# Performance work log

Measured on AMD Instinct MI355X. Metric: run time of the kernel, lower is better.

The kernel has to match this reference:

```python
import jax, jax.numpy as jnp
import numpy as np

B, N = 4, 2466  # batch, vertex count (Pixel2Mesh stage-3 mesh)
IMG = 224.0


def _vertex_align(feat_maps, pos):
    """Bilinear-style gather of image features at projected vertex locations.
    feat_maps: list of [B,C,S,S]; pos: [B,N,3]. Returns [B,N,sum(C)]."""
    z = pos[..., 2]
    h = jnp.clip(248.0 * (pos[..., 1] / z) + 111.5, 0.0, 223.0)
    w = jnp.clip(248.0 * (pos[..., 0] / (-z)) + 111.5, 0.0, 223.0)
    outs = []
    for f in feat_maps:
        S = f.shape[-1]
        x = h / (IMG / S)
        y = w / (IMG / S)
        x1 = jnp.floor(x).astype(jnp.int32)
        x2 = jnp.minimum(jnp.ceil(x).astype(jnp.int32), S - 1)
        y1 = jnp.floor(y).astype(jnp.int32)
        y2 = jnp.minimum(jnp.ceil(y).astype(jnp.int32), S - 1)
        xi = x.astype(jnp.int32)  # trunc == floor since x >= 0
        yi = y.astype(jnp.int32)

        def gat(fm, xs, ys):  # fm [C,S,S], xs/ys [N] -> [N,C]
            return fm[:, xs, ys].T

        g = jax.vmap(gat)
        w11 = ((x2 - xi) * (y2 - yi)).astype(f.dtype)[..., None]
        w12 = ((x2 - xi) * (yi - y1)).astype(f.dtype)[..., None]
        w21 = ((xi - x1) * (y2 - yi)).astype(f.dtype)[..., None]
        w22 = ((xi - x1) * (yi - y1)).astype(f.dtype)[..., None]
        outs.append(w11 * g(f, x1, y1) + w21 * g(f, x2, y1)
                    + w12 * g(f, x1, y2) + w22 * g(f, x2, y2))
    return jnp.concatenate(outs, axis=-1)


def _graph_conv(x, adj, w0, w1):
    # relu(X @ w0 + A @ (X @ w1))
    return jax.nn.relu(x @ w0 + jnp.einsum('bmn,bnc->bmc', adj, x @ w1))


def _res_graph_conv(x, adj, pw, pb, w00, w01, w10, w11):
    skip = x @ pw + pb
    out = _graph_conv(x, adj, w00, w01)
    out = _graph_conv(out, adj, w10, w11)
    return skip + out


def _forward(conv2_3, conv3_4, conv4_6, conv5_3, vertex_positions, vertex_features,
             vertex_adjacency, lin_w, lin_b,
             r0_pw, r0_pb, r0_w00, r0_w01, r0_w10, r0_w11,
             r1_pw, r1_pb, r1_w00, r1_w01, r1_w10, r1_w11,
             r2_pw, r2_pb, r2_w00, r2_w01, r2_w10, r2_w11,
             gf_w0, gf_w1):
    aligned = _vertex_align([conv2_3, conv3_4, conv4_6, conv5_3], vertex_positions)  # [B,N,3840]
    proj = aligned @ lin_w + lin_b  # [B,N,128]
    x = jnp.concatenate([proj, vertex_features, vertex_positions], axis=-1)  # [B,N,259]
    x = _res_graph_conv(x, vertex_adjacency, r0_pw, r0_pb, r0_w00, r0_w01, r0_w10, r0_w11)
    x = _res_graph_conv(x, vertex_adjacency, r1_pw, r1_pb, r1_w00, r1_w01, r1_w10, r1_w11)
    x = _res_graph_conv(x, vertex_adjacency, r2_pw, r2_pb, r2_w00, r2_w01, r2_w10, r2_w11)
    offset = jnp.tanh(_graph_conv(x, vertex_adjacency, gf_w0, gf_w1))  # [B,N,3]
    return vertex_positions + offset


def setup_inputs() -> dict:
    key = jax.random.key(0)
    ks = jax.random.split(key, 40)
    inp = {
        "conv2_3": jax.random.normal(ks[0], (B, 256, 56, 56), jnp.float32),
        "conv3_4": jax.random.normal(ks[1], (B, 512, 28, 28), jnp.float32),
        "conv4_6": jax.random.normal(ks[2], (B, 1024, 14, 14), jnp.float32),
        "conv5_3": jax.random.normal(ks[3], (B, 2048, 7, 7), jnp.float32),
        "vertex_positions": jax.random.normal(ks[4], (B, N, 3), jnp.float32),
        "vertex_features": jax.random.normal(ks[5], (B, N, 128), jnp.float32),
        # sparse 0/1 adjacency stored dense (the torch module uses dense bmm)
        "vertex_adjacency": (jax.random.uniform(ks[6], (B, N, N)) < 0.003).astype(jnp.float32),
    }

    def u(k, shape, fan):
        b = 1.0 / np.sqrt(fan)
        return jax.random.uniform(k, shape, jnp.float32, -b, b)

    specs = [("lin_w", (3840, 128), 3840), ("lin_b", (128,), 3840)]
    for j, ci in enumerate([259, 128, 128]):
        p = f"r{j}_"
        specs += [(p + "pw", (ci, 128), ci), (p + "pb", (128,), ci),
                  (p + "w00", (ci, 128), ci), (p + "w01", (ci, 128), ci),
                  (p + "w10", (128, 128), 128), (p + "w11", (128, 128), 128)]
    specs += [("gf_w0", (128, 3), 128), ("gf_w1", (128, 3), 128)]
    for i, (name, shape, fan) in enumerate(specs):
        inp[name] = u(ks[7 + i], shape, fan)
    return inp


def reference(conv2_3, conv3_4, conv4_6, conv5_3, vertex_positions, vertex_features,
              vertex_adjacency, lin_w, lin_b,
              r0_pw, r0_pb, r0_w00, r0_w01, r0_w10, r0_w11,
              r1_pw, r1_pb, r1_w00, r1_w01, r1_w10, r1_w11,
              r2_pw, r2_pb, r2_w00, r2_w01, r2_w10, r2_w11,
              gf_w0, gf_w1):
    return _forward(conv2_3, conv3_4, conv4_6, conv5_3, vertex_positions, vertex_features,
                    vertex_adjacency, lin_w, lin_b,
                    r0_pw, r0_pb, r0_w00, r0_w01, r0_w10, r0_w11,
                    r1_pw, r1_pb, r1_w00, r1_w01, r1_w10, r1_w11,
                    r2_pw, r2_pb, r2_w00, r2_w01, r2_w10, r2_w11,
                    gf_w0, gf_w1)
```

## Files before the change

### kernel.cpp

```cpp
#include <hip/hip_runtime.h>
#include <cmath>

#define B_   4
#define N_   2466
#define R_   (B_*N_)
#define ELLW 96

typedef _Float16 f16x8 __attribute__((ext_vector_type(8)));
typedef _Float16 f16x4 __attribute__((ext_vector_type(4)));
typedef __attribute__((ext_vector_type(4))) float f32x4;

__device__ __forceinline__ unsigned short f16_bits(float x) {
  union { _Float16 h; unsigned short u; } c;
  c.h = (_Float16)x;
  return c.u;
}

struct WMats { const float* p[15]; };


__global__ __launch_bounds__(256) void k_pre(
    const float* __restrict__ c2, const float* __restrict__ c3,
    const float* __restrict__ c4, const float* __restrict__ c5,
    unsigned short* __restrict__ t0, unsigned short* __restrict__ t1,
    unsigned short* __restrict__ t2, unsigned short* __restrict__ t3,
    const float* __restrict__ adj, int* __restrict__ cols, int* __restrict__ cnts,
    const float* __restrict__ lin_w,
    unsigned short* __restrict__ whf,
    WMats wm,
    unsigned short* __restrict__ wrf) {
  __shared__ float t[64][66];
  int bid = blockIdx.x;
  int tid = threadIdx.x;
  if (bid < 1584) {
    const float* in; unsigned short* out; int C, P, npb, ncb, rem;
    if (bid < 784)       { in = c2; out = t0; C = 256;  P = 3136; npb = 49; ncb = 4;  rem = bid; }
    else if (bid < 1200) { in = c3; out = t1; C = 512;  P = 784;  npb = 13; ncb = 8;  rem = bid - 784; }
    else if (bid < 1456) { in = c4; out = t2; C = 1024; P = 196;  npb = 4;  ncb = 16; rem = bid - 1200; }
    else                 { in = c5; out = t3; C = 2048; P = 49;   npb = 1;  ncb = 32; rem = bid - 1456; }
    int pb = rem % npb; int tq = rem / npb; int cb = tq % ncb; int b = tq / ncb;
    int c0 = cb * 64, p0 = pb * 64;
    #pragma unroll
    for (int i = 0; i < 8; i++) {
      int e = tid + i * 256;
      int c = e >> 5, f2 = e & 31;
      int p = p0 + f2 * 2;
      float2 v = make_float2(0.f, 0.f);
      const float* src = in + ((size_t)b * C + (c0 + c)) * P + p;
      if (p + 1 < P)      v = *(const float2*)src;
      else if (p < P)     v.x = *src;
      *(float2*)&t[c][f2 * 2] = v;
    }
    __syncthreads();
    int jj = tid & 15, c4i = jj * 4;
    #pragma unroll
    for (int pass = 0; pass < 4; pass++) {
      int pp = pass * 16 + (tid >> 4);
      int px = p0 + pp;
      if (px < P) {
        ushort4 o;
        o.x = f16_bits(t[c4i + 0][pp]);
        o.y = f16_bits(t[c4i + 1][pp]);
        o.z = f16_bits(t[c4i + 2][pp]);
        o.w = f16_bits(t[c4i + 3][pp]);
        *(ushort4*)&out[((size_t)b * P + px) * C + c0 + c4i] = o;
      }
    }
  } else if (bid < 4050) {
    int wave = tid >> 6, lane = tid & 63;
    int row = (bid - 1584) * 4 + wave;
    const float* Ar = adj + (size_t)row * N_;
    int* cp = cols + (size_t)row * ELLW;
    unsigned long long below = (lane == 63) ? 0xFFFFFFFFFFFFFFFFull >> 1
                                            : ((1ull << lane) - 1ull);
    float4 v[10];
    #pragma unroll
    for (int i0 = 0; i0 < 10; i0++) {
      int j0 = i0 * 256 + lane * 4;
      if (j0 + 3 < N_) {
        v[i0] = *(const float4*)&Ar[j0];
      } else {
        v[i0] = make_float4(0.f, 0.f, 0.f, 0.f);
        if (j0     < N_) v[i0].x = Ar[j0];
        if (j0 + 1 < N_) v[i0].y = Ar[j0+1];
        if (j0 + 2 < N_) v[i0].z = Ar[j0+2];
      }
    }
    int base = 0;
    #pragma unroll
    for (int i0 = 0; i0 < 10; i0++) {
      int j0 = i0 * 256 + lane * 4;
      bool nz0 = (j0     < N_) && (v[i0].x != 0.f);
      bool nz1 = (j0 + 1 < N_) && (v[i0].y != 0.f);
      bool nz2 = (j0 + 2 < N_) && (v[i0].z != 0.f);
      bool nz3 = (j0 + 3 < N_) && (v[i0].w != 0.f);
      unsigned long long m0 = __ballot(nz0);
      unsigned long long m1 = __ballot(nz1);
      unsigned long long m2 = __ballot(nz2);
      unsigned long long m3 = __ballot(nz3);
      int pre = __popcll(m0 & below) + __popcll(m1 & below)
              + __popcll(m2 & below) + __popcll(m3 & below);
      int p0 = base + pre;
      int p1 = p0 + (nz0 ? 1 : 0);
      int p2 = p1 + (nz1 ? 1 : 0);
      int p3 = p2 + (nz2 ? 1 : 0);
      if (nz0 && p0 < ELLW) cp[p0] = j0;
      if (nz1 && p1 < ELLW) cp[p1] = j0 + 1;
      if (nz2 && p2 < ELLW) cp[p2] = j0 + 2;
      if (nz3 && p3 < ELLW) cp[p3] = j0 + 3;
      base += __popcll(m0) + __popcll(m1) + __popcll(m2) + __popcll(m3);
    }
    if (lane == 0) cnts[row] = (base > ELLW) ? ELLW : base;
  } else if (bid < 4530) {
    int b = bid - 4050;
    int e0 = (b * 256 + tid) * 4;
    #pragma unroll
    for (int u = 0; u < 4; u++) {
      int e = e0 + u;
      int j = e & 7;
      int lane = (e >> 3) & 63;
      int nt = (e >> 9) & 7;
      int slab = e >> 12;
      int k = slab * 32 + ((lane >> 4) << 3) + j;
      int n = nt * 16 + (lane & 15);
      whf[e] = f16_bits(lin_w[(size_t)k * 128 + n]);
    }
  } else {
    int b = bid - 4530;
    int e0 = (b * 256 + tid) * 4;
    #pragma unroll
    for (int u = 0; u < 4; u++) {
      int e = e0 + u;
      int rb, mat, rem, K;
      if (e < 143360) {
        rb = 0;
        if (e < 110592) { mat = e / 36864; rem = e - mat * 36864; K = 259; }
        else { int tt = e - 110592; mat = 3 + tt / 16384; rem = tt & 16383; K = 128; }
      } else {
        int tt = e - 143360;
        rb = 1 + tt / 81920;
        int r2 = tt % 81920;
        mat = r2 / 16384; rem = r2 & 16383; K = 128;
      }
      int j = rem & 7, lane = (rem >> 3) & 63, nt = (rem >> 9) & 7, slab = rem >> 12;
      int k = slab * 32 + ((lane >> 4) << 3) + j;
      int n = nt * 16 + (lane & 15);
      float x = (k < K) ? wm.p[rb * 5 + mat][(size_t)k * 128 + n] : 0.f;
      wrf[e] = f16_bits(x);
    }
  }
}

__global__ __launch_bounds__(256) void k_align_mfma(
    const unsigned short* __restrict__ tr0, const unsigned short* __restrict__ tr1,
    const unsigned short* __restrict__ tr2, const unsigned short* __restrict__ tr3,
    const float* __restrict__ pos,
    const unsigned short* __restrict__ whf,
    unsigned short* __restrict__ part, int kchunk) {
  int tid  = threadIdx.x;
  int wave = tid >> 6, lane = tid & 63;
  int q    = lane >> 4, l15 = lane & 15;
  int m0   = blockIdx.x * 128;
  int s    = blockIdx.y;

  int zero[2][4]; int base[2][4];
  #pragma unroll
  for (int u = 0; u < 2; u++) {
    int mrow = m0 + (wave * 2 + u) * 16 + l15;
    int rowc = (mrow < R_) ? mrow : 0;
    int b = rowc / N_;
    float px = pos[rowc*3+0], py = pos[rowc*3+1], pz = pos[rowc*3+2];
    float hh = fminf(fmaxf(248.f*(py/pz)    + 111.5f, 0.f), 223.f);
    float wc = fminf(fmaxf(248.f*(px/(-pz)) + 111.5f, 0.f), 223.f);
    const int Sarr[4] = {56, 28, 14, 7};
    const int Carr[4] = {256, 512, 1024, 2048};
    #pragma unroll
    for (int sc = 0; sc < 4; sc++) {
      int S = Sarr[sc], C = Carr[sc];
      float dv = 224.f / (float)S;
      float x = hh / dv, y = wc / dv;
      int x1 = (int)floorf(x), y1 = (int)floorf(y);
      int x2 = min((int)ceilf(x), S - 1), y2 = min((int)ceilf(y), S - 1);
      int w = (x2 - x1) * (y2 - y1);
      zero[u][sc] = (mrow >= R_) || (w == 0);
      base[u][sc] = (b * S * S + x1 * S + y1) * C;
    }
  }

  f32x4 acc[2][8];
  #pragma unroll
  for (int u = 0; u < 2; u++)
    #pragma unroll
    for (int nt = 0; nt < 8; nt++) acc[u][nt] = (f32x4){0.f, 0.f, 0.f, 0.f};

  const f16x8* BH = (const f16x8*)whf;

  int kbeg = s * kchunk, kend = kbeg + kchunk;
  #pragma unroll 1
  for (int k0 = kbeg; k0 < kend; k0 += 32) {
    const unsigned short* tr; int off, sI;
    if (k0 < 256)       { tr = tr0; off = 0;    sI = 0; }
    else if (k0 < 768)  { tr = tr1; off = 256;  sI = 1; }
    else if (k0 < 1792) { tr = tr2; off = 768;  sI = 2; }
    else                { tr = tr3; off = 1792; sI = 3; }

    f16x8 af[2];
    #pragma unroll
    for (int u = 0; u < 2; u++) {
      af[u] = *(const f16x8*)(tr + base[u][sI] + (k0 - off) + q * 8);
      if (zero[u][sI]) af[u] = (f16x8)(_Float16)0;
    }

    int slab = k0 >> 5;
    f16x8 Bh[8];
    #pragma unroll
    for (int nt = 0; nt < 8; nt++)
      Bh[nt] = BH[(size_t)(slab * 8 + nt) * 64 + lane];
    #pragma unroll
    for (int nt = 0; nt < 8; nt++) {
      acc[0][nt] = __builtin_amdgcn_mfma_f32_16x16x32_f16(af[0], Bh[nt], acc[0][nt], 0, 0, 0);
      acc[1][nt] = __builtin_amdgcn_mfma_f32_16x16x32_f16(af[1], Bh[nt], acc[1][nt], 0, 0, 0);
    }
  }

  #pragma unroll
  for (int u = 0; u < 2; u++)
    #pragma unroll
    for (int nt = 0; nt < 8; nt++)
      #pragma unroll
      for (int r = 0; r < 4; r++) {
        int row = m0 + (wave * 2 + u) * 16 + q * 4 + r;
        if (row < R_)
          part[((size_t)s * R_ + row) * 128 + nt * 16 + l15] = f16_bits(acc[u][nt][r]);
      }
}

__global__ __launch_bounds__(256) void k_reduce(
    const unsigned short* __restrict__ part, const float* __restrict__ lin_b,
    const float* __restrict__ vf, const float* __restrict__ pos,
    unsigned short* __restrict__ xcat, int nsplit) {
  int grp = threadIdx.x >> 5, ln = threadIdx.x & 31;
  int row = blockIdx.x * 8 + grp;
  float4 acc = ((const float4*)lin_b)[ln];
  const f16x4* p4 = (const f16x4*)part;
  for (int s = 0; s < nsplit; s++) {
    f16x4 pv = p4[((size_t)s * R_ + row) * 32 + ln];
    acc.x += (float)pv[0]; acc.y += (float)pv[1];
    acc.z += (float)pv[2]; acc.w += (float)pv[3];
  }
  ushort4* xr = (ushort4*)(xcat + (size_t)row * 288);
  ushort4 o;
  o.x = f16_bits(acc.x); o.y = f16_bits(acc.y);
  o.z = f16_bits(acc.z); o.w = f16_bits(acc.w);
  xr[ln] = o;
  float4 vv = ((const float4*)vf)[(size_t)row * 32 + ln];
  o.x = f16_bits(vv.x); o.y = f16_bits(vv.y);
  o.z = f16_bits(vv.z); o.w = f16_bits(vv.w);
  xr[32 + ln] = o;
  if (ln < 8) {
    ushort4 z = make_ushort4(0, 0, 0, 0);
    if (ln == 0) {
      z.x = f16_bits(pos[(size_t)row * 3 + 0]);
      z.y = f16_bits(pos[(size_t)row * 3 + 1]);
      z.z = f16_bits(pos[(size_t)row * 3 + 2]);
    }
    xr[64 + ln] = z;
  }
}

template<int SLABS>
__global__ __launch_bounds__(256) void k_gemm_mfma(
    const unsigned short* __restrict__ X, int ldx,
    const unsigned short* __restrict__ wf,
    int matStride, const float* __restrict__ pb,
    unsigned short* __restrict__ o0, unsigned short* __restrict__ o1,
    unsigned short* __restrict__ o2) {
  int tid = threadIdx.x;
  int wave = tid >> 6, lane = tid & 63;
  int q = lane >> 4, l15 = lane & 15;
  int which = blockIdx.y;
  int m0 = blockIdx.x * 64;
  int mrow = m0 + wave * 16 + l15;
  int rowc = (mrow < R_) ? mrow : (R_ - 1);
  const unsigned short* xrow = X + (size_t)rowc * ldx + q * 8;

  const f16x8* BH = (const f16x8*)(wf + (size_t)which * matStride);

  f32x4 acc[8];
  #pragma unroll
  for (int nt = 0; nt < 8; nt++) acc[nt] = (f32x4){0.f, 0.f, 0.f, 0.f};

  #pragma unroll 1
  for (int slab = 0; slab < SLABS; slab++) {
    f16x8 af = *(const f16x8*)(xrow + slab * 32);
    f16x8 Bh[8];
    #pragma unroll
    for (int nt = 0; nt < 8; nt++)
      Bh[nt] = BH[(size_t)(slab * 8 + nt) * 64 + lane];
    #pragma unroll
    for (int nt = 0; nt < 8; nt++)
      acc[nt] = __builtin_amdgcn_mfma_f32_16x16x32_f16(af, Bh[nt], acc[nt], 0, 0, 0);
  }

  unsigned short* out = (which == 0) ? o0 : (which == 1) ? o1 : o2;
  #pragma unroll
  for (int nt = 0; nt < 8; nt++) {
    int col = nt * 16 + l15;
    float bias = (pb != nullptr && which == 2) ? pb[col] : 0.f;
    #pragma unroll
    for (int r = 0; r < 4; r++) {
      int row = m0 + wave * 16 + q * 4 + r;
      if (row < R_) out[(size_t)row * 128 + col] = f16_bits(acc[nt][r] + bias);
    }
  }
}

__global__ __launch_bounds__(256) void k_spmm(
    const unsigned short* __restrict__ sb, const unsigned short* __restrict__ tb,
    const int* __restrict__ cols, const int* __restrict__ cnts,
    const unsigned short* __restrict__ skipb, unsigned short* __restrict__ outb,
    const float* __restrict__ gw0, const float* __restrict__ gw1,
    unsigned short* __restrict__ gsb, unsigned short* __restrict__ gtb, int fuse_gf) {
  int tid = threadIdx.x;
  int grp = tid >> 5, ln = tid & 31;
  int row = blockIdx.x * 8 + grp;
  int b = row / N_;
  size_t tbase = (size_t)b * N_;
  const f16x4* sb4 = (const f16x4*)sb;
  const f16x4* tb4 = (const f16x4*)tb;
  const int* cp = cols + (size_t)row * ELLW;
  int4 ci0 = *(const int4*)cp;
  int4 ci1 = *(const int4*)(cp + 4);
  int4 ci2 = *(const int4*)(cp + 8);
  int cnt = cnts[row];
  f16x4 sv = sb4[(size_t)row*32 + ln];
  float4 acc = make_float4((float)sv[0], (float)sv[1], (float)sv[2], (float)sv[3]);
  int idx[12] = {ci0.x, ci0.y, ci0.z, ci0.w, ci1.x, ci1.y, ci1.z, ci1.w,
                 ci2.x, ci2.y, ci2.z, ci2.w};
  f16x4 g[12];
  #pragma unroll
  for (int i = 0; i < 12; i++) {
    int c = idx[i];
    c = (c >= 0 && c < N_) ? c : 0;
    g[i] = tb4[(tbase + c)*32 + ln];
  }
  #pragma unroll
  for (int i = 0; i < 12; i++) {
    if (i < cnt) {
      acc.x += (float)g[i][0]; acc.y += (float)g[i][1];
      acc.z += (float)g[i][2]; acc.w += (float)g[i][3];
    }
  }
  for (int i = 12; i < cnt; i++) {
    f16x4 v = tb4[(tbase + cp[i])*32 + ln];
    acc.x += (float)v[0]; acc.y += (float)v[1];
    acc.z += (float)v[2]; acc.w += (float)v[3];
  }
  acc.x = fmaxf(acc.x, 0.f); acc.y = fmaxf(acc.y, 0.f);
  acc.z = fmaxf(acc.z, 0.f); acc.w = fmaxf(acc.w, 0.f);
  if (skipb) {
    f16x4 sk = ((const f16x4*)skipb)[(size_t)row*32 + ln];
    acc.x += (float)sk[0]; acc.y += (float)sk[1];
    acc.z += (float)sk[2]; acc.w += (float)sk[3];
  }
  if (!fuse_gf) {
    ushort4 o;
    o.x = f16_bits(acc.x); o.y = f16_bits(acc.y);
    o.z = f16_bits(acc.z); o.w = f16_bits(acc.w);
    ((ushort4*)outb)[(size_t)row*32 + ln] = o;
    return;
  }
  float av[4] = {acc.x, acc.y, acc.z, acc.w};
  int j0 = ln * 4;
  float p0 = 0.f, p1 = 0.f, p2 = 0.f, q0 = 0.f, q1 = 0.f, q2 = 0.f;
  #pragma unroll
  for (int u = 0; u < 4; u++) {
    int j = j0 + u;
    p0 += av[u] * gw0[j*3+0]; p1 += av[u] * gw0[j*3+1]; p2 += av[u] * gw0[j*3+2];
    q0 += av[u] * gw1[j*3+0]; q1 += av[u] * gw1[j*3+1]; q2 += av[u] * gw1[j*3+2];
  }
  #pragma unroll
  for (int off = 16; off >= 1; off >>= 1) {
    p0 += __shfl_xor(p0, off); p1 += __shfl_xor(p1, off); p2 += __shfl_xor(p2, off);
    q0 += __shfl_xor(q0, off); q1 += __shfl_xor(q1, off); q2 += __shfl_xor(q2, off);
  }
  if (ln == 0) {
    gsb[(size_t)row*128 + 0] = f16_bits(p0);
    gsb[(size_t)row*128 + 1] = f16_bits(p1);
    gsb[(size_t)row*128 + 2] = f16_bits(p2);
    gtb[(size_t)row*128 + 0] = f16_bits(q0);
    gtb[(size_t)row*128 + 1] = f16_bits(q1);
    gtb[(size_t)row*128 + 2] = f16_bits(q2);
  }
}

__global__ __launch_bounds__(256) void k_gf_final(
    const unsigned short* __restrict__ sb, const unsigned short* __restrict__ tb,
    const int* __restrict__ cols, const int* __restrict__ cnts,
    const float* __restrict__ pos, float* __restrict__ out) {
  int wave = threadIdx.x >> 6, lane = threadIdx.x & 63;
  int row = blockIdx.x * 4 + wave;
  if (lane >= 3) return;
  int b = row / N_;
  size_t tbase = (size_t)b * N_;
  const int* cp = cols + (size_t)row * ELLW;
  int4 ci0 = *(const int4*)cp;
  int4 ci1 = *(const int4*)(cp + 4);
  int4 ci2 = *(const int4*)(cp + 8);
  int cnt = cnts[row];
  union { unsigned short u; _Float16 h; } cv;
  cv.u = sb[(size_t)row*128 + lane];
  float acc = (float)cv.h;
  int idx[12] = {ci0.x, ci0.y, ci0.z, ci0.w, ci1.x, ci1.y, ci1.z, ci1.w,
                 ci2.x, ci2.y, ci2.z, ci2.w};
  float g[12];
  #pragma unroll
  for (int i = 0; i < 12; i++) {
    int c = idx[i];
    c = (c >= 0 && c < N_) ? c : 0;
    cv.u = tb[(tbase + c)*128 + lane];
    g[i] = (float)cv.h;
  }
  #pragma unroll
  for (int i = 0; i < 12; i++)
    if (i < cnt) acc += g[i];
  for (int i = 12; i < cnt; i++) {
    cv.u = tb[(tbase + cp[i])*128 + lane];
    acc += (float)cv.h;
  }
  float v = tanhf(fmaxf(acc, 0.f));
  out[(size_t)row*3 + lane] = pos[(size_t)row*3 + lane] + v;
}

extern "C" void kernel_launch(void* const* d_in, const int* in_sizes, int n_in,
                              void* d_out, int out_size, void* d_ws, size_t ws_size,
                              hipStream_t stream) {
  const float* conv2_3 = (const float*)d_in[0];
  const float* conv3_4 = (const float*)d_in[1];
  const float* conv4_6 = (const float*)d_in[2];
  const float* conv5_3 = (const float*)d_in[3];
  const float* pos     = (const float*)d_in[4];
  const float* vf      = (const float*)d_in[5];
  const float* adj     = (const float*)d_in[6];
  const float* lin_w   = (const float*)d_in[7];
  const float* lin_b   = (const float*)d_in[8];
  const float* r_pb[3]  = {(const float*)d_in[10], (const float*)d_in[16], (const float*)d_in[22]};
  const float* gf_w0 = (const float*)d_in[27];
  const float* gf_w1 = (const float*)d_in[28];
  float* out = (float*)d_out;

  const size_t ROWF    = (size_t)R_ * 128;
  const size_t XCATE   = (size_t)R_ * 288;
  const size_t LINW_E  = 491520;
  const size_t RESW_E  = 307200;

  unsigned short* trh0 = (unsigned short*)d_ws;
  unsigned short* trh1 = trh0 + (size_t)4*256*3136;
  unsigned short* trh2 = trh1 + (size_t)4*512*784;
  unsigned short* trh3 = trh2 + (size_t)4*1024*196;
  int*   ell_cnt  = (int*)(trh3 + (size_t)4*2048*49);
  int*   ell_cols = ell_cnt + R_;
  unsigned short* whf = (unsigned short*)(ell_cols + (size_t)R_*ELLW);
  unsigned short* wrf = whf + LINW_E;
  unsigned short* part = wrf + RESW_E + 512;

  size_t fixed_h = 6021120 + 2*(size_t)R_*(ELLW+1) + LINW_E + RESW_E + 512;
  size_t need8 = (fixed_h + (size_t)8*ROWF + XCATE + 5*ROWF + 1024) * 2;
  int nsplit = (ws_size >= need8) ? 8 : 4;
  int kchunk = 3840 / nsplit;

  unsigned short* xcat = part + (size_t)nsplit * ROWF;
  unsigned short* sb   = xcat + XCATE;
  unsigned short* tb   = sb   + ROWF;
  unsigned short* skip = tb   + ROWF;
  unsigned short* hb   = skip + ROWF;
  unsigned short* xc   = hb   + ROWF;

  WMats wm;
  for (int rb = 0; rb < 3; rb++) {
    wm.p[rb*5 + 0] = (const float*)d_in[11 + 6*rb];
    wm.p[rb*5 + 1] = (const float*)d_in[12 + 6*rb];
    wm.p[rb*5 + 2] = (const float*)d_in[9  + 6*rb];
    wm.p[rb*5 + 3] = (const float*)d_in[13 + 6*rb];
    wm.p[rb*5 + 4] = (const float*)d_in[14 + 6*rb];
  }
  const int RB_BASE[3] = {0, 143360, 225280};

  k_pre<<<4830, 256, 0, stream>>>(conv2_3, conv3_4, conv4_6, conv5_3,
                                  trh0, trh1, trh2, trh3,
                                  adj, ell_cols, ell_cnt,
                                  lin_w, whf, wm, wrf);

  k_align_mfma<<<dim3(78, nsplit), 256, 0, stream>>>(trh0, trh1, trh2, trh3, pos,
                                                     whf, part, kchunk);

  k_reduce<<<1233, 256, 0, stream>>>(part, lin_b, vf, pos, xcat, nsplit);

  for (int rb = 0; rb < 3; rb++) {
    if (rb == 0) {
      k_gemm_mfma<9><<<dim3(155, 3), 256, 0, stream>>>(
          xcat, 288, wrf + RB_BASE[0], 36864, r_pb[0], sb, tb, skip);
    } else {
      k_gemm_mfma<4><<<dim3(155, 3), 256, 0, stream>>>(
          xc, 128, wrf + RB_BASE[rb], 16384, r_pb[rb], sb, tb, skip);
    }
    k_spmm<<<1233, 256, 0, stream>>>(sb, tb, ell_cols, ell_cnt, nullptr, hb,
                                     nullptr, nullptr, nullptr, nullptr, 0);
    int g2off = RB_BASE[rb] + ((rb == 0) ? 110592 : 3 * 16384);
    k_gemm_mfma<4><<<dim3(155, 2), 256, 0, stream>>>(
        hb, 128, wrf + g2off, 16384, nullptr, sb, tb, nullptr);
    if (rb < 2) {
      k_spmm<<<1233, 256, 0, stream>>>(sb, tb, ell_cols, ell_cnt, skip, xc,
                                       nullptr, nullptr, nullptr, nullptr, 0);
    } else {
      k_spmm<<<1233, 256, 0, stream>>>(sb, tb, ell_cols, ell_cnt, skip, nullptr,
                                       gf_w0, gf_w1, hb, xc, 1);
    }
  }

  k_gf_final<<<2466, 256, 0, stream>>>(hb, xc, ell_cols, ell_cnt, pos, out);
}
```

Before: 379.7 us.

## Fuse post-preprocess kernels into one persistent megakernel with grid barriers

Replaces the sequence of align, reduce, gemm, spmm and final kernels with a single persistent kernel of 768 blocks. The blocks loop over virtual block indices for each phase and synchronise with a software grid barrier built on atomics. The aim is to remove roughly fifteen kernel launch gaps and the tail drain at each boundary. In exchange it relies on all 768 blocks being co-resident, since the launch bounds are set for 3 blocks per CU; otherwise the barrier can deadlock, which is only softened by a spin timeout. The spmm and final phases also lose some parallelism, and the megakernel may carry higher register pressure.

Result: slower. 1.506 ms (+296.6%).

```diff
diff --git a/kernel.cpp b/kernel.cpp
--- a/kernel.cpp
+++ b/kernel.cpp
@@ -5,6 +5,7 @@
 #define N_   2466
 #define R_   (B_*N_)
 #define ELLW 96
+#define GRID_MEGA 768
 
 typedef _Float16 f16x8 __attribute__((ext_vector_type(8)));
 typedef _Float16 f16x4 __attribute__((ext_vector_type(4)));
@@ -28,10 +29,12 @@
     const float* __restrict__ lin_w,
     unsigned short* __restrict__ whf,
     WMats wm,
-    unsigned short* __restrict__ wrf) {
+    unsigned short* __restrict__ wrf,
+    unsigned int* __restrict__ bar) {
   __shared__ float t[64][66];
   int bid = blockIdx.x;
   int tid = threadIdx.x;
+  if (bid == 0 && tid == 0) { bar[0] = 0u; bar[1] = 0u; }
   if (bid < 1584) {
     const float* in; unsigned short* out; int C, P, npb, ncb, rem;
     if (bid < 784)       { in = c2; out = t0; C = 256;  P = 3136; npb = 49; ncb = 4;  rem = bid; }
@@ -151,17 +154,37 @@
   }
 }
 
-__global__ __launch_bounds__(256) void k_align_mfma(
+__device__ __forceinline__ void gridbar(unsigned int* bar) {
+  __syncthreads();
+  if (threadIdx.x == 0) {
+    unsigned int gen = __hip_atomic_load(&bar[1], __ATOMIC_RELAXED, __HIP_MEMORY_SCOPE_AGENT);
+    unsigned int a = __hip_atomic_fetch_add(&bar[0], 1u, __ATOMIC_ACQ_REL, __HIP_MEMORY_SCOPE_AGENT);
+    if (a == GRID_MEGA - 1u) {
+      __hip_atomic_store(&bar[0], 0u, __ATOMIC_RELAXED, __HIP_MEMORY_SCOPE_AGENT);
+      __hip_atomic_fetch_add(&bar[1], 1u, __ATOMIC_ACQ_REL, __HIP_MEMORY_SCOPE_AGENT);
+    } else {
+      int spins = 0;
+      while (__hip_atomic_load(&bar[1], __ATOMIC_RELAXED, __HIP_MEMORY_SCOPE_AGENT) == gen) {
+        __builtin_amdgcn_s_sleep(2);
+        if (++spins > (1 << 24)) break;
+      }
+      __builtin_amdgcn_fence(__ATOMIC_ACQUIRE, "agent");
+    }
+  }
+  __syncthreads();
+}
+
+
+__device__ __forceinline__ void phase_align(int vb,
     const unsigned short* __restrict__ tr0, const unsigned short* __restrict__ tr1,
     const unsigned short* __restrict__ tr2, const unsigned short* __restrict__ tr3,
-    const float* __restrict__ pos,
-    const unsigned short* __restrict__ whf,
+    const float* __restrict__ pos, const unsigned short* __restrict__ whf,
     unsigned short* __restrict__ part, int kchunk) {
   int tid  = threadIdx.x;
   int wave = tid >> 6, lane = tid & 63;
   int q    = lane >> 4, l15 = lane & 15;
-  int m0   = blockIdx.x * 128;
-  int s    = blockIdx.y;
+  int s    = vb / 78;
+  int m0   = (vb - s * 78) * 128;
 
   int zero[2][4]; int base[2][4];
   #pragma unroll
@@ -235,12 +258,12 @@
       }
 }
 
-__global__ __launch_bounds__(256) void k_reduce(
+__device__ __forceinline__ void phase_reduce(int vb,
     const unsigned short* __restrict__ part, const float* __restrict__ lin_b,
     const float* __restrict__ vf, const float* __restrict__ pos,
     unsigned short* __restrict__ xcat, int nsplit) {
   int grp = threadIdx.x >> 5, ln = threadIdx.x & 31;
-  int row = blockIdx.x * 8 + grp;
+  int row = vb * 8 + grp;
   float4 acc = ((const float4*)lin_b)[ln];
   const f16x4* p4 = (const f16x4*)part;
   for (int s = 0; s < nsplit; s++) {
@@ -268,18 +291,16 @@
   }
 }
 
-template<int SLABS>
-__global__ __launch_bounds__(256) void k_gemm_mfma(
+__device__ __forceinline__ void phase_gemm(int vb,
     const unsigned short* __restrict__ X, int ldx,
-    const unsigned short* __restrict__ wf,
-    int matStride, const float* __restrict__ pb,
+    const unsigned short* __restrict__ wf, int matStride, const float* __restrict__ pb,
     unsigned short* __restrict__ o0, unsigned short* __restrict__ o1,
-    unsigned short* __restrict__ o2) {
+    unsigned short* __restrict__ o2, int slabs) {
   int tid = threadIdx.x;
   int wave = tid >> 6, lane = tid & 63;
   int q = lane >> 4, l15 = lane & 15;
-  int which = blockIdx.y;
-  int m0 = blockIdx.x * 64;
+  int which = vb / 155;
+  int m0 = (vb - which * 155) * 64;
   int mrow = m0 + wave * 16 + l15;
   int rowc = (mrow < R_) ? mrow : (R_ - 1);
   const unsigned short* xrow = X + (size_t)rowc * ldx + q * 8;
@@ -291,7 +312,7 @@
   for (int nt = 0; nt < 8; nt++) acc[nt] = (f32x4){0.f, 0.f, 0.f, 0.f};
 
   #pragma unroll 1
-  for (int slab = 0; slab < SLABS; slab++) {
+  for (int slab = 0; slab < slabs; slab++) {
     f16x8 af = *(const f16x8*)(xrow + slab * 32);
     f16x8 Bh[8];
     #pragma unroll
@@ -315,7 +336,7 @@
   }
 }
 
-__global__ __launch_bounds__(256) void k_spmm(
+__device__ __forceinline__ void phase_spmm(int vb,
     const unsigned short* __restrict__ sb, const unsigned short* __restrict__ tb,
     const int* __restrict__ cols, const int* __restrict__ cnts,
     const unsigned short* __restrict__ skipb, unsigned short* __restrict__ outb,
@@ -323,7 +344,7 @@
     unsigned short* __restrict__ gsb, unsigned short* __restrict__ gtb, int fuse_gf) {
   int tid = threadIdx.x;
   int grp = tid >> 5, ln = tid & 31;
-  int row = blockIdx.x * 8 + grp;
+  int row = vb * 8 + grp;
   int b = row / N_;
   size_t tbase = (size_t)b * N_;
   const f16x4* sb4 = (const f16x4*)sb;
@@ -394,13 +415,13 @@
   }
 }
 
-__global__ __launch_bounds__(256) void k_gf_final(
-    const unsigned short* __restrict__ sb, const unsigned short* __restrict__ tb,
+__device__ __forceinline__ void phase_final(int vb,
+    const unsigned short* __restrict__ sbuf, const unsigned short* __restrict__ tbuf,
     const int* __restrict__ cols, const int* __restrict__ cnts,
     const float* __restrict__ pos, float* __restrict__ out) {
-  int wave = threadIdx.x >> 6, lane = threadIdx.x & 63;
-  int row = blockIdx.x * 4 + wave;
-  if (lane >= 3) return;
+  int grp = threadIdx.x >> 5, ln = threadIdx.x & 31;
+  int row = vb * 8 + grp;
+  if (ln >= 3) return;
   int b = row / N_;
   size_t tbase = (size_t)b * N_;
   const int* cp = cols + (size_t)row * ELLW;
@@ -409,7 +430,7 @@
   int4 ci2 = *(const int4*)(cp + 8);
   int cnt = cnts[row];
   union { unsigned short u; _Float16 h; } cv;
-  cv.u = sb[(size_t)row*128 + lane];
+  cv.u = sbuf[(size_t)row*128 + ln];
   float acc = (float)cv.h;
   int idx[12] = {ci0.x, ci0.y, ci0.z, ci0.w, ci1.x, ci1.y, ci1.z, ci1.w,
                  ci2.x, ci2.y, ci2.z, ci2.w};
@@ -418,18 +439,81 @@
   for (int i = 0; i < 12; i++) {
     int c = idx[i];
     c = (c >= 0 && c < N_) ? c : 0;
-    cv.u = tb[(tbase + c)*128 + lane];
+    cv.u = tbuf[(tbase + c)*128 + ln];
     g[i] = (float)cv.h;
   }
   #pragma unroll
   for (int i = 0; i < 12; i++)
     if (i < cnt) acc += g[i];
   for (int i = 12; i < cnt; i++) {
-    cv.u = tb[(tbase + cp[i])*128 + lane];
+    cv.u = tbuf[(tbase + cp[i])*128 + ln];
     acc += (float)cv.h;
   }
   float v = tanhf(fmaxf(acc, 0.f));
-  out[(size_t)row*3 + lane] = pos[(size_t)row*3 + lane] + v;
+  out[(size_t)row*3 + ln] = pos[(size_t)row*3 + ln] + v;
+}
+
+__global__ __launch_bounds__(256, 3) void k_mega(
+    const unsigned short* __restrict__ tr0, const unsigned short* __restrict__ tr1,
+    const unsigned short* __restrict__ tr2, const unsigned short* __restrict__ tr3,
+    const float* __restrict__ pos, const unsigned short* __restrict__ whf,
+    unsigned short* __restrict__ part, int kchunk, int nsplit,
+    const float* __restrict__ lin_b, const float* __restrict__ vf,
+    unsigned short* __restrict__ xcat, const unsigned short* __restrict__ wrf,
+    const float* __restrict__ pb0, const float* __restrict__ pb1, const float* __restrict__ pb2,
+    unsigned short* __restrict__ sb, unsigned short* __restrict__ tb,
+    unsigned short* __restrict__ skip, unsigned short* __restrict__ hb,
+    unsigned short* __restrict__ xc,
+    const int* __restrict__ cols, const int* __restrict__ cnts,
+    const float* __restrict__ gw0, const float* __restrict__ gw1,
+    float* __restrict__ out, unsigned int* __restrict__ bar) {
+  const int bid = blockIdx.x;
+
+  for (int vb = bid; vb < 78 * nsplit; vb += GRID_MEGA)
+    phase_align(vb, tr0, tr1, tr2, tr3, pos, whf, part, kchunk);
+  gridbar(bar);
+
+  for (int vb = bid; vb < 1233; vb += GRID_MEGA)
+    phase_reduce(vb, part, lin_b, vf, pos, xcat, nsplit);
+  gridbar(bar);
+
+  #pragma unroll
+  for (int rb = 0; rb < 3; rb++) {
+    const unsigned short* X = (rb == 0) ? xcat : xc;
+    const int ldx    = (rb == 0) ? 288 : 128;
+    const int slabs  = (rb == 0) ? 9 : 4;
+    const int base   = (rb == 0) ? 0 : ((rb == 1) ? 143360 : 225280);
+    const int mstr   = (rb == 0) ? 36864 : 16384;
+    const float* pb  = (rb == 0) ? pb0 : ((rb == 1) ? pb1 : pb2);
+
+    for (int vb = bid; vb < 155 * 3; vb += GRID_MEGA)
+      phase_gemm(vb, X, ldx, wrf + base, mstr, pb, sb, tb, skip, slabs);
+    gridbar(bar);
+
+    for (int vb = bid; vb < 1233; vb += GRID_MEGA)
+      phase_spmm(vb, sb, tb, cols, cnts, nullptr, hb,
+                 nullptr, nullptr, nullptr, nullptr, 0);
+    gridbar(bar);
+
+    const int g2off = base + ((rb == 0) ? 110592 : 3 * 16384);
+    for (int vb = bid; vb < 155 * 2; vb += GRID_MEGA)
+      phase_gemm(vb, hb, 128, wrf + g2off, 16384, nullptr, sb, tb, nullptr, 4);
+    gridbar(bar);
+
+    if (rb < 2) {
+      for (int vb = bid; vb < 1233; vb += GRID_MEGA)
+        phase_spmm(vb, sb, tb, cols, cnts, skip, xc,
+                   nullptr, nullptr, nullptr, nullptr, 0);
+    } else {
+      for (int vb = bid; vb < 1233; vb += GRID_MEGA)
+        phase_spmm(vb, sb, tb, cols, cnts, skip, nullptr,
+                   gw0, gw1, hb, xc, 1);
+    }
+    gridbar(bar);
+  }
+
+  for (int vb = bid; vb < 1233; vb += GRID_MEGA)
+    phase_final(vb, hb, xc, cols, cnts, pos, out);
 }
 
 extern "C" void kernel_launch(void* const* d_in, const int* in_sizes, int n_in,
@@ -462,6 +546,7 @@
   int*   ell_cols = ell_cnt + R_;
   unsigned short* whf = (unsigned short*)(ell_cols + (size_t)R_*ELLW);
   unsigned short* wrf = whf + LINW_E;
+  unsigned int*   bar = (unsigned int*)(wrf + RESW_E);
   unsigned short* part = wrf + RESW_E + 512;
 
   size_t fixed_h = 6021120 + 2*(size_t)R_*(ELLW+1) + LINW_E + RESW_E + 512;
@@ -484,39 +569,15 @@
     wm.p[rb*5 + 3] = (const float*)d_in[13 + 6*rb];
     wm.p[rb*5 + 4] = (const float*)d_in[14 + 6*rb];
   }
-  const int RB_BASE[3] = {0, 143360, 225280};
 
   k_pre<<<4830, 256, 0, stream>>>(conv2_3, conv3_4, conv4_6, conv5_3,
                                   trh0, trh1, trh2, trh3,
                                   adj, ell_cols, ell_cnt,
-                                  lin_w, whf, wm, wrf);
-
-  k_align_mfma<<<dim3(78, nsplit), 256, 0, stream>>>(trh0, trh1, trh2, trh3, pos,
-                                                     whf, part, kchunk);
-
-  k_reduce<<<1233, 256, 0, stream>>>(part, lin_b, vf, pos, xcat, nsplit);
-
-  for (int rb = 0; rb < 3; rb++) {
-    if (rb == 0) {
-      k_gemm_mfma<9><<<dim3(155, 3), 256, 0, stream>>>(
-          xcat, 288, wrf + RB_BASE[0], 36864, r_pb[0], sb, tb, skip);
-    } else {
-      k_gemm_mfma<4><<<dim3(155, 3), 256, 0, stream>>>(
-          xc, 128, wrf + RB_BASE[rb], 16384, r_pb[rb], sb, tb, skip);
-    }
-    k_spmm<<<1233, 256, 0, stream>>>(sb, tb, ell_cols, ell_cnt, nullptr, hb,
-                                     nullptr, nullptr, nullptr, nullptr, 0);
-    int g2off = RB_BASE[rb] + ((rb == 0) ? 110592 : 3 * 16384);
-    k_gemm_mfma<4><<<dim3(155, 2), 256, 0, stream>>>(
-        hb, 128, wrf + g2off, 16384, nullptr, sb, tb, nullptr);
-    if (rb < 2) {
-      k_spmm<<<1233, 256, 0, stream>>>(sb, tb, ell_cols, ell_cnt, skip, xc,
-                                       nullptr, nullptr, nullptr, nullptr, 0);
-    } else {
-      k_spmm<<<1233, 256, 0, stream>>>(sb, tb, ell_cols, ell_cnt, skip, nullptr,
-                                       gf_w0, gf_w1, hb, xc, 1);
-    }
-  }
-
-  k_gf_final<<<2466, 256, 0, stream>>>(hb, xc, ell_cols, ell_cnt, pos, out);
-}
+                                  lin_w, whf, wm, wrf, bar);
+
+  k_mega<<<GRID_MEGA, 256, 0, stream>>>(trh0, trh1, trh2, trh3, pos, whf, part,
+                                        kchunk, nsplit, lin_b, vf, xcat, wrf,
+                                        r_pb[0], r_pb[1], r_pb[2],
+                                        sb, tb, skip, hb, xc,
+                                        ell_cols, ell_cnt, gf_w0, gf_w1, out, bar);
+}
```

## Fuse split-K reduce and sparse adjacency aggregation into GEMM A-operand prologue

Applied to the files above, without the earlier changes.

Replaces the separate reduce kernel and most SpMM kernels with a templated GEMM that builds its A tile on the fly. In mode 0 it sums the split-K partials plus bias and converts vertex features and positions. In mode 1 it gathers ELL neighbours, applies ReLU and adds the skip term before the MFMA loop. This removes several launches and intermediate round-trips through global memory. In exchange, the neighbour gather is recomputed redundantly in each of the 2–3 output-matrix blocks (blockIdx.y), and holding all A fragments in registers raises register pressure.

Measured after the change: 439.2 us. 15.7% more time.

```diff
diff --git a/kernel.cpp b/kernel.cpp
--- a/kernel.cpp
+++ b/kernel.cpp
@@ -235,44 +235,15 @@
       }
 }
 
-__global__ __launch_bounds__(256) void k_reduce(
+template<int MODE, int SLABS>
+__global__ __launch_bounds__(256) void k_ggemm(
+    const unsigned short* __restrict__ s_in,
+    const unsigned short* __restrict__ t_in,
+    const unsigned short* __restrict__ skip_in,
+    const int* __restrict__ cols, const int* __restrict__ cnts,
     const unsigned short* __restrict__ part, const float* __restrict__ lin_b,
-    const float* __restrict__ vf, const float* __restrict__ pos,
-    unsigned short* __restrict__ xcat, int nsplit) {
-  int grp = threadIdx.x >> 5, ln = threadIdx.x & 31;
-  int row = blockIdx.x * 8 + grp;
-  float4 acc = ((const float4*)lin_b)[ln];
-  const f16x4* p4 = (const f16x4*)part;
-  for (int s = 0; s < nsplit; s++) {
-    f16x4 pv = p4[((size_t)s * R_ + row) * 32 + ln];
-    acc.x += (float)pv[0]; acc.y += (float)pv[1];
-    acc.z += (float)pv[2]; acc.w += (float)pv[3];
-  }
-  ushort4* xr = (ushort4*)(xcat + (size_t)row * 288);
-  ushort4 o;
-  o.x = f16_bits(acc.x); o.y = f16_bits(acc.y);
-  o.z = f16_bits(acc.z); o.w = f16_bits(acc.w);
-  xr[ln] = o;
-  float4 vv = ((const float4*)vf)[(size_t)row * 32 + ln];
-  o.x = f16_bits(vv.x); o.y = f16_bits(vv.y);
-  o.z = f16_bits(vv.z); o.w = f16_bits(vv.w);
-  xr[32 + ln] = o;
-  if (ln < 8) {
-    ushort4 z = make_ushort4(0, 0, 0, 0);
-    if (ln == 0) {
-      z.x = f16_bits(pos[(size_t)row * 3 + 0]);
-      z.y = f16_bits(pos[(size_t)row * 3 + 1]);
-      z.z = f16_bits(pos[(size_t)row * 3 + 2]);
-    }
-    xr[64 + ln] = z;
-  }
-}
-
-template<int SLABS>
-__global__ __launch_bounds__(256) void k_gemm_mfma(
-    const unsigned short* __restrict__ X, int ldx,
-    const unsigned short* __restrict__ wf,
-    int matStride, const float* __restrict__ pb,
+    const float* __restrict__ vf, const float* __restrict__ pos, int nsplit,
+    const unsigned short* __restrict__ wf, int matStride, const float* __restrict__ pb,
     unsigned short* __restrict__ o0, unsigned short* __restrict__ o1,
     unsigned short* __restrict__ o2) {
   int tid = threadIdx.x;
@@ -282,24 +253,111 @@
   int m0 = blockIdx.x * 64;
   int mrow = m0 + wave * 16 + l15;
   int rowc = (mrow < R_) ? mrow : (R_ - 1);
-  const unsigned short* xrow = X + (size_t)rowc * ldx + q * 8;
+
+  f16x8 af[SLABS];
+  if constexpr (MODE == 0) {
+    #pragma unroll
+    for (int slab = 0; slab < 4; slab++) {
+      int kof = slab * 32 + q * 8;
+      float4 b0 = *(const float4*)&lin_b[kof];
+      float4 b1 = *(const float4*)&lin_b[kof + 4];
+      float a8[8] = {b0.x, b0.y, b0.z, b0.w, b1.x, b1.y, b1.z, b1.w};
+      for (int s = 0; s < nsplit; s++) {
+        f16x8 pv = *(const f16x8*)&part[((size_t)s * R_ + rowc) * 128 + kof];
+        #pragma unroll
+        for (int j = 0; j < 8; j++) a8[j] += (float)pv[j];
+      }
+      f16x8 a;
+      #pragma unroll
+      for (int j = 0; j < 8; j++) a[j] = (_Float16)a8[j];
+      af[slab] = a;
+    }
+    #pragma unroll
+    for (int slab = 4; slab < 8; slab++) {
+      int kof = (slab - 4) * 32 + q * 8;
+      float4 v0 = *(const float4*)&vf[(size_t)rowc * 128 + kof];
+      float4 v1 = *(const float4*)&vf[(size_t)rowc * 128 + kof + 4];
+      f16x8 a;
+      a[0] = (_Float16)v0.x; a[1] = (_Float16)v0.y;
+      a[2] = (_Float16)v0.z; a[3] = (_Float16)v0.w;
+      a[4] = (_Float16)v1.x; a[5] = (_Float16)v1.y;
+      a[6] = (_Float16)v1.z; a[7] = (_Float16)v1.w;
+      af[slab] = a;
+    }
+    {
+      f16x8 a = (f16x8)(_Float16)0;
+      if (q == 0) {
+        a[0] = (_Float16)pos[(size_t)rowc * 3 + 0];
+        a[1] = (_Float16)pos[(size_t)rowc * 3 + 1];
+        a[2] = (_Float16)pos[(size_t)rowc * 3 + 2];
+      }
+      af[SLABS - 1] = a;
+    }
+  } else {
+    const int* cp = cols + (size_t)rowc * ELLW;
+    int4 ci0 = *(const int4*)cp;
+    int4 ci1 = *(const int4*)(cp + 4);
+    int4 ci2 = *(const int4*)(cp + 8);
+    int cnt = cnts[rowc];
+    size_t tbase = (size_t)(rowc / N_) * N_;
+    int idx[12] = {ci0.x, ci0.y, ci0.z, ci0.w, ci1.x, ci1.y, ci1.z, ci1.w,
+                   ci2.x, ci2.y, ci2.z, ci2.w};
+    #pragma unroll
+    for (int i = 0; i < 12; i++) {
+      int c = idx[i];
+      idx[i] = (c >= 0 && c < N_) ? c : 0;
+    }
+    #pragma unroll
+    for (int slab = 0; slab < SLABS; slab++) {
+      int kof = slab * 32 + q * 8;
+      f16x8 sv = *(const f16x8*)&s_in[(size_t)rowc * 128 + kof];
+      float a8[8];
+      #pragma unroll
+      for (int j = 0; j < 8; j++) a8[j] = (float)sv[j];
+      f16x8 g[12];
+      #pragma unroll
+      for (int i = 0; i < 12; i++)
+        g[i] = *(const f16x8*)&t_in[(tbase + idx[i]) * 128 + kof];
+      #pragma unroll
+      for (int i = 0; i < 12; i++) {
+        if (i < cnt) {
+          #pragma unroll
+          for (int j = 0; j < 8; j++) a8[j] += (float)g[i][j];
+        }
+      }
+      for (int i = 12; i < cnt; i++) {
+        f16x8 v = *(const f16x8*)&t_in[(tbase + cp[i]) * 128 + kof];
+        #pragma unroll
+        for (int j = 0; j < 8; j++) a8[j] += (float)v[j];
+      }
+      #pragma unroll
+      for (int j = 0; j < 8; j++) a8[j] = fmaxf(a8[j], 0.f);
+      if (skip_in) {
+        f16x8 sk = *(const f16x8*)&skip_in[(size_t)rowc * 128 + kof];
+        #pragma unroll
+        for (int j = 0; j < 8; j++) a8[j] += (float)sk[j];
+      }
+      f16x8 a;
+      #pragma unroll
+      for (int j = 0; j < 8; j++) a[j] = (_Float16)a8[j];
+      af[slab] = a;
+    }
+  }
 
   const f16x8* BH = (const f16x8*)(wf + (size_t)which * matStride);
-
   f32x4 acc[8];
   #pragma unroll
   for (int nt = 0; nt < 8; nt++) acc[nt] = (f32x4){0.f, 0.f, 0.f, 0.f};
 
-  #pragma unroll 1
+  #pragma unroll
   for (int slab = 0; slab < SLABS; slab++) {
-    f16x8 af = *(const f16x8*)(xrow + slab * 32);
     f16x8 Bh[8];
     #pragma unroll
     for (int nt = 0; nt < 8; nt++)
       Bh[nt] = BH[(size_t)(slab * 8 + nt) * 64 + lane];
     #pragma unroll
     for (int nt = 0; nt < 8; nt++)
-      acc[nt] = __builtin_amdgcn_mfma_f32_16x16x32_f16(af, Bh[nt], acc[nt], 0, 0, 0);
+      acc[nt] = __builtin_amdgcn_mfma_f32_16x16x32_f16(af[slab], Bh[nt], acc[nt], 0, 0, 0);
   }
 
   unsigned short* out = (which == 0) ? o0 : (which == 1) ? o1 : o2;
@@ -450,7 +508,6 @@
   float* out = (float*)d_out;
 
   const size_t ROWF    = (size_t)R_ * 128;
-  const size_t XCATE   = (size_t)R_ * 288;
   const size_t LINW_E  = 491520;
   const size_t RESW_E  = 307200;
 
@@ -465,16 +522,18 @@
   unsigned short* part = wrf + RESW_E + 512;
 
   size_t fixed_h = 6021120 + 2*(size_t)R_*(ELLW+1) + LINW_E + RESW_E + 512;
-  size_t need8 = (fixed_h + (size_t)8*ROWF + XCATE + 5*ROWF + 1024) * 2;
+  size_t need8 = (fixed_h + (size_t)8*ROWF + 8*ROWF + 1024) * 2;
   int nsplit = (ws_size >= need8) ? 8 : 4;
   int kchunk = 3840 / nsplit;
 
-  unsigned short* xcat = part + (size_t)nsplit * ROWF;
-  unsigned short* sb   = xcat + XCATE;
+  unsigned short* sb   = part + (size_t)nsplit * ROWF;
   unsigned short* tb   = sb   + ROWF;
-  unsigned short* skip = tb   + ROWF;
-  unsigned short* hb   = skip + ROWF;
-  unsigned short* xc   = hb   + ROWF;
+  unsigned short* sb2  = tb   + ROWF;
+  unsigned short* tb2  = sb2  + ROWF;
+  unsigned short* skA  = tb2  + ROWF;
+  unsigned short* skB  = skA  + ROWF;
+  unsigned short* gsb  = skB  + ROWF;
+  unsigned short* gtb  = gsb  + ROWF;
 
   WMats wm;
   for (int rb = 0; rb < 3; rb++) {
@@ -484,7 +543,6 @@
     wm.p[rb*5 + 3] = (const float*)d_in[13 + 6*rb];
     wm.p[rb*5 + 4] = (const float*)d_in[14 + 6*rb];
   }
-  const int RB_BASE[3] = {0, 143360, 225280};
 
   k_pre<<<4830, 256, 0, stream>>>(conv2_3, conv3_4, conv4_6, conv5_3,
                                   trh0, trh1, trh2, trh3,
@@ -494,29 +552,38 @@
   k_align_mfma<<<dim3(78, nsplit), 256, 0, stream>>>(trh0, trh1, trh2, trh3, pos,
                                                      whf, part, kchunk);
 
-  k_reduce<<<1233, 256, 0, stream>>>(part, lin_b, vf, pos, xcat, nsplit);
-
-  for (int rb = 0; rb < 3; rb++) {
-    if (rb == 0) {
-      k_gemm_mfma<9><<<dim3(155, 3), 256, 0, stream>>>(
-          xcat, 288, wrf + RB_BASE[0], 36864, r_pb[0], sb, tb, skip);
-    } else {
-      k_gemm_mfma<4><<<dim3(155, 3), 256, 0, stream>>>(
-          xc, 128, wrf + RB_BASE[rb], 16384, r_pb[rb], sb, tb, skip);
-    }
-    k_spmm<<<1233, 256, 0, stream>>>(sb, tb, ell_cols, ell_cnt, nullptr, hb,
-                                     nullptr, nullptr, nullptr, nullptr, 0);
-    int g2off = RB_BASE[rb] + ((rb == 0) ? 110592 : 3 * 16384);
-    k_gemm_mfma<4><<<dim3(155, 2), 256, 0, stream>>>(
-        hb, 128, wrf + g2off, 16384, nullptr, sb, tb, nullptr);
-    if (rb < 2) {
-      k_spmm<<<1233, 256, 0, stream>>>(sb, tb, ell_cols, ell_cnt, skip, xc,
-                                       nullptr, nullptr, nullptr, nullptr, 0);
-    } else {
-      k_spmm<<<1233, 256, 0, stream>>>(sb, tb, ell_cols, ell_cnt, skip, nullptr,
-                                       gf_w0, gf_w1, hb, xc, 1);
-    }
-  }
-
-  k_gf_final<<<2466, 256, 0, stream>>>(hb, xc, ell_cols, ell_cnt, pos, out);
-}
+  k_ggemm<0,9><<<dim3(155, 3), 256, 0, stream>>>(
+      nullptr, nullptr, nullptr, ell_cols, ell_cnt,
+      part, lin_b, vf, pos, nsplit,
+      wrf + 0, 36864, r_pb[0], sb, tb, skA);
+
+  k_ggemm<1,4><<<dim3(155, 2), 256, 0, stream>>>(
+      sb, tb, nullptr, ell_cols, ell_cnt,
+      nullptr, nullptr, nullptr, nullptr, 0,
+      wrf + 110592, 16384, nullptr, sb2, tb2, nullptr);
+
+  k_ggemm<1,4><<<dim3(155, 3), 256, 0, stream>>>(
+      sb2, tb2, skA, ell_cols, ell_cnt,
+      nullptr, nullptr, nullptr, nullptr, 0,
+      wrf + 143360, 16384, r_pb[1], sb, tb, skB);
+
+  k_ggemm<1,4><<<dim3(155, 2), 256, 0, stream>>>(
+      sb, tb, nullptr, ell_cols, ell_cnt,
+      nullptr, nullptr, nullptr, nullptr, 0,
+      wrf + 192512, 16384, nullptr, sb2, tb2, nullptr);
+
+  k_ggemm<1,4><<<dim3(155, 3), 256, 0, stream>>>(
+      sb2, tb2, skB, ell_cols, ell_cnt,
+      nullptr, nullptr, nullptr, nullptr, 0,
+      wrf + 225280, 16384, r_pb[2], sb, tb, skA);
+
+  k_ggemm<1,4><<<dim3(155, 2), 256, 0, stream>>>(
+      sb, tb, nullptr, ell_cols, ell_cnt,
+      nullptr, nullptr, nullptr, nullptr, 0,
+      wrf + 274432, 16384, nullptr, sb2, tb2, nullptr);
+
+  k_spmm<<<1233, 256, 0, stream>>>(sb2, tb2, ell_cols, ell_cnt, skA, nullptr,
+                                   gf_w0, gf_w1, gsb, gtb, 1);
+
+  k_gf_final<<<2466, 256, 0, stream>>>(gsb, gtb, ell_cols, ell_cnt, pos, out);
+}
```

## Fuse sparse adjacency aggregation with following graph-conv GEMM per row tile

Applied to the files above, without the earlier changes.

Adds a k_fuse kernel that computes the ELL SpMM aggregation (plus relu and optional skip) for a 32-row tile into shared memory, then immediately runs the next layer's MFMA GEMMs on that tile. The residual block chain becomes a sequence of fused launches with ping-pong buffers, so the intermediate hidden activation is never written to and re-read from global memory and several launches disappear. The cost is that each block also loads the full weight slabs for only 32 rows, and the workspace requirement grows by three row buffers.

New measurement: 380.1 us. About the same (+0.1%).

```diff
diff --git a/kernel.cpp b/kernel.cpp
--- a/kernel.cpp
+++ b/kernel.cpp
@@ -311,6 +311,109 @@
     for (int r = 0; r < 4; r++) {
       int row = m0 + wave * 16 + q * 4 + r;
       if (row < R_) out[(size_t)row * 128 + col] = f16_bits(acc[nt][r] + bias);
+    }
+  }
+}
+
+template<int NW>
+__global__ __launch_bounds__(256) void k_fuse(
+    const unsigned short* __restrict__ s_in,
+    const unsigned short* __restrict__ t_in,
+    const unsigned short* __restrict__ skip_in,
+    const int* __restrict__ cols, const int* __restrict__ cnts,
+    const unsigned short* __restrict__ wf, const float* __restrict__ pb,
+    unsigned short* __restrict__ o0, unsigned short* __restrict__ o1,
+    unsigned short* __restrict__ o2) {
+  __shared__ unsigned short hsm[32][136];
+  int tid = threadIdx.x;
+  int r0 = blockIdx.x * 32;
+
+  {
+    int grp = tid >> 5, ln = tid & 31;
+    const f16x4* s4 = (const f16x4*)s_in;
+    const f16x4* t4 = (const f16x4*)t_in;
+    #pragma unroll 1
+    for (int rr = 0; rr < 4; rr++) {
+      int lrow = grp * 4 + rr;
+      int row = r0 + lrow;
+      int rowc = (row < R_) ? row : (R_ - 1);
+      int b = rowc / N_;
+      size_t tbase = (size_t)b * N_;
+      const int* cp = cols + (size_t)rowc * ELLW;
+      int4 ci0 = *(const int4*)cp;
+      int4 ci1 = *(const int4*)(cp + 4);
+      int4 ci2 = *(const int4*)(cp + 8);
+      int cnt = cnts[rowc];
+      f16x4 sv = s4[(size_t)rowc*32 + ln];
+      float4 acc = make_float4((float)sv[0], (float)sv[1], (float)sv[2], (float)sv[3]);
+      int idx[12] = {ci0.x, ci0.y, ci0.z, ci0.w, ci1.x, ci1.y, ci1.z, ci1.w,
+                     ci2.x, ci2.y, ci2.z, ci2.w};
+      f16x4 g[12];
+      #pragma unroll
+      for (int i = 0; i < 12; i++) {
+        int c = idx[i];
+        c = (c >= 0 && c < N_) ? c : 0;
+        g[i] = t4[(tbase + c)*32 + ln];
+      }
+      #pragma unroll
+      for (int i = 0; i < 12; i++) {
+        if (i < cnt) {
+          acc.x += (float)g[i][0]; acc.y += (float)g[i][1];
+          acc.z += (float)g[i][2]; acc.w += (float)g[i][3];
+        }
+      }
+      for (int i = 12; i < cnt; i++) {
+        f16x4 v = t4[(tbase + cp[i])*32 + ln];
+        acc.x += (float)v[0]; acc.y += (float)v[1];
+        acc.z += (float)v[2]; acc.w += (float)v[3];
+      }
+      acc.x = fmaxf(acc.x, 0.f); acc.y = fmaxf(acc.y, 0.f);
+      acc.z = fmaxf(acc.z, 0.f); acc.w = fmaxf(acc.w, 0.f);
+      if (skip_in) {
+        f16x4 sk = ((const f16x4*)skip_in)[(size_t)rowc*32 + ln];
+        acc.x += (float)sk[0]; acc.y += (float)sk[1];
+        acc.z += (float)sk[2]; acc.w += (float)sk[3];
+      }
+      ushort4 o;
+      o.x = f16_bits(acc.x); o.y = f16_bits(acc.y);
+      o.z = f16_bits(acc.z); o.w = f16_bits(acc.w);
+      *(ushort4*)&hsm[lrow][ln * 4] = o;
+    }
+  }
+  __syncthreads();
+
+  int wave = tid >> 6, lane = tid & 63;
+  int q = lane >> 4, l15 = lane & 15;
+  int mt = wave & 1, nh = wave >> 1;
+  const unsigned short* xrow = &hsm[mt * 16 + l15][q * 8];
+
+  #pragma unroll 1
+  for (int which = 0; which < NW; which++) {
+    const f16x8* BH = (const f16x8*)(wf + (size_t)which * 16384);
+    f32x4 acc[4];
+    #pragma unroll
+    for (int t2 = 0; t2 < 4; t2++) acc[t2] = (f32x4){0.f, 0.f, 0.f, 0.f};
+    #pragma unroll
+    for (int slab = 0; slab < 4; slab++) {
+      f16x8 af = *(const f16x8*)(xrow + slab * 32);
+      f16x8 Bh[4];
+      #pragma unroll
+      for (int t2 = 0; t2 < 4; t2++)
+        Bh[t2] = BH[(size_t)(slab * 8 + nh * 4 + t2) * 64 + lane];
+      #pragma unroll
+      for (int t2 = 0; t2 < 4; t2++)
+        acc[t2] = __builtin_amdgcn_mfma_f32_16x16x32_f16(af, Bh[t2], acc[t2], 0, 0, 0);
+    }
+    unsigned short* out = (which == 0) ? o0 : (which == 1) ? o1 : o2;
+    #pragma unroll
+    for (int t2 = 0; t2 < 4; t2++) {
+      int col = (nh * 4 + t2) * 16 + l15;
+      float bias = (pb != nullptr && which == 2) ? pb[col] : 0.f;
+      #pragma unroll
+      for (int r = 0; r < 4; r++) {
+        int row = r0 + mt * 16 + q * 4 + r;
+        if (row < R_) out[(size_t)row * 128 + col] = f16_bits(acc[t2][r] + bias);
+      }
     }
   }
 }
@@ -465,16 +568,19 @@
   unsigned short* part = wrf + RESW_E + 512;
 
   size_t fixed_h = 6021120 + 2*(size_t)R_*(ELLW+1) + LINW_E + RESW_E + 512;
-  size_t need8 = (fixed_h + (size_t)8*ROWF + XCATE + 5*ROWF + 1024) * 2;
+  size_t need8 = (fixed_h + (size_t)8*ROWF + XCATE + 8*ROWF + 1024) * 2;
   int nsplit = (ws_size >= need8) ? 8 : 4;
   int kchunk = 3840 / nsplit;
 
   unsigned short* xcat = part + (size_t)nsplit * ROWF;
   unsigned short* sb   = xcat + XCATE;
   unsigned short* tb   = sb   + ROWF;
-  unsigned short* skip = tb   + ROWF;
-  unsigned short* hb   = skip + ROWF;
-  unsigned short* xc   = hb   + ROWF;
+  unsigned short* sb2  = tb   + ROWF;
+  unsigned short* tb2  = sb2  + ROWF;
+  unsigned short* skA  = tb2  + ROWF;
+  unsigned short* skB  = skA  + ROWF;
+  unsigned short* gsb  = skB  + ROWF;
+  unsigned short* gtb  = gsb  + ROWF;
 
   WMats wm;
   for (int rb = 0; rb < 3; rb++) {
@@ -484,7 +590,8 @@
     wm.p[rb*5 + 3] = (const float*)d_in[13 + 6*rb];
     wm.p[rb*5 + 4] = (const float*)d_in[14 + 6*rb];
   }
-  const int RB_BASE[3] = {0, 143360, 225280};
+
+  const int NFB = (R_ + 31) / 32;
 
   k_pre<<<4830, 256, 0, stream>>>(conv2_3, conv3_4, conv4_6, conv5_3,
                                   trh0, trh1, trh2, trh3,
@@ -496,27 +603,26 @@
 
   k_reduce<<<1233, 256, 0, stream>>>(part, lin_b, vf, pos, xcat, nsplit);
 
-  for (int rb = 0; rb < 3; rb++) {
-    if (rb == 0) {
-      k_gemm_mfma<9><<<dim3(155, 3), 256, 0, stream>>>(
-          xcat, 288, wrf + RB_BASE[0], 36864, r_pb[0], sb, tb, skip);
-    } else {
-      k_gemm_mfma<4><<<dim3(155, 3), 256, 0, stream>>>(
-          xc, 128, wrf + RB_BASE[rb], 16384, r_pb[rb], sb, tb, skip);
-    }
-    k_spmm<<<1233, 256, 0, stream>>>(sb, tb, ell_cols, ell_cnt, nullptr, hb,
-                                     nullptr, nullptr, nullptr, nullptr, 0);
-    int g2off = RB_BASE[rb] + ((rb == 0) ? 110592 : 3 * 16384);
-    k_gemm_mfma<4><<<dim3(155, 2), 256, 0, stream>>>(
-        hb, 128, wrf + g2off, 16384, nullptr, sb, tb, nullptr);
-    if (rb < 2) {
-      k_spmm<<<1233, 256, 0, stream>>>(sb, tb, ell_cols, ell_cnt, skip, xc,
-                                       nullptr, nullptr, nullptr, nullptr, 0);
-    } else {
-      k_spmm<<<1233, 256, 0, stream>>>(sb, tb, ell_cols, ell_cnt, skip, nullptr,
-                                       gf_w0, gf_w1, hb, xc, 1);
-    }
-  }
-
-  k_gf_final<<<2466, 256, 0, stream>>>(hb, xc, ell_cols, ell_cnt, pos, out);
-}
+  k_gemm_mfma<9><<<dim3(155, 3), 256, 0, stream>>>(
+      xcat, 288, wrf + 0, 36864, r_pb[0], sb, tb, skA);
+
+  k_fuse<2><<<NFB, 256, 0, stream>>>(sb, tb, nullptr, ell_cols, ell_cnt,
+                                     wrf + 110592, nullptr, sb2, tb2, nullptr);
+
+  k_fuse<3><<<NFB, 256, 0, stream>>>(sb2, tb2, skA, ell_cols, ell_cnt,
+                                     wrf + 143360, r_pb[1], sb, tb, skB);
+
+  k_fuse<2><<<NFB, 256, 0, stream>>>(sb, tb, nullptr, ell_cols, ell_cnt,
+                                     wrf + 192512, nullptr, sb2, tb2, nullptr);
+
+  k_fuse<3><<<NFB, 256, 0, stream>>>(sb2, tb2, skB, ell_cols, ell_cnt,
+                                     wrf + 225280, r_pb[2], sb, tb, skA);
+
+  k_fuse<2><<<NFB, 256, 0, stream>>>(sb, tb, nullptr, ell_cols, ell_cnt,
+                                     wrf + 274432, nullptr, sb2, tb2, nullptr);
+
+  k_spmm<<<1233, 256, 0, stream>>>(sb2, tb2, ell_cols, ell_cnt, skA, nullptr,
+                                   gf_w0, gf_w1, gsb, gtb, 1);
+
+  k_gf_final<<<2466, 256, 0, stream>>>(gsb, gtb, ell_cols, ell_cnt, pos, out);
+}
```
